# Kernel optimization log

Hardware: AMD Instinct MI355X
Metric: run time of the kernel (lower is better)

## Reference

```python
import jax, jax.numpy as jnp
import numpy as np

BATCH, DIM = 32, 512
STDDEV = 0.1


def _annihilation(dim):
    # diag(sqrt(1..dim-1), k=1), complex64
    d = jnp.sqrt(jnp.arange(1, dim, dtype=jnp.float32)).astype(jnp.complex64)
    return jnp.diag(d, k=1)


def setup_inputs() -> dict:
    key = jax.random.key(0)
    ks = jax.random.split(key, 8)
    f = lambda k, shape: jax.random.normal(k, shape, dtype=jnp.float32)
    return {
        'inputs_re': f(ks[0], (BATCH, DIM, DIM)),
        'inputs_im': f(ks[1], (BATCH, DIM, DIM)),
        'theta_1': f(ks[2], (1,)) * STDDEV,
        'theta_2': f(ks[3], (1,)) * STDDEV,
        'r': f(ks[4], (1,)) * STDDEV,
        'bx': f(ks[5], (1,)) * STDDEV,
        'bp': f(ks[6], (1,)) * STDDEV,
        'kappa': f(ks[7], (1,)) * STDDEV,
    }


def _forward(inputs_re, inputs_im, theta_1, theta_2, r, bx, bp, kappa):
    dim = inputs_re.shape[-1]
    x = jax.lax.complex(inputs_re, inputs_im)  # [B, dim, dim] complex64

    a = _annihilation(dim)                     # [dim, dim]
    a_dag = a.conj().T
    n_diag = jnp.arange(dim, dtype=jnp.float32).astype(jnp.complex64)  # number-operator diagonal

    # Rotation operators: expm(-1i*theta*N) with N diagonal -> closed-form diagonal exp (same math)
    th1 = theta_1[0].astype(jnp.complex64)
    th2 = theta_2[0].astype(jnp.complex64)
    R1 = jnp.diag(jnp.exp(-1j * th1 * n_diag))
    R2 = jnp.diag(jnp.exp(-1j * th2 * n_diag))

    # Kerr operator: expm(1i*kappa * (N*N elementwise)) ; N diagonal so N*N = diag(k^2)
    kap = kappa[0].astype(jnp.complex64)
    K = jnp.diag(jnp.exp(1j * kap * n_diag * n_diag))

    # Squeezing: in the TF source, '*' is ELEMENTWISE, and adjoint(a) (subdiag) elementwise
    # times a (superdiag) is the zero matrix -> generator is identically 0 -> S = expm(0) = I.
    # We keep the (zero) generator in the graph so r stays a (zero-grad) primal.
    r_c = r[0].astype(jnp.complex64)
    M_S = 0.5 * (r_c * (a_dag * a) - jnp.conj(r_c) * (a * a_dag))  # exactly zeros
    S = jnp.eye(dim, dtype=jnp.complex64) + M_S

    # Displacement: D = expm(alpha*a_dag - conj(alpha)*a). Generator M is skew-Hermitian,
    # so M = iH with H = -iM Hermitian; D = V diag(exp(i*w)) V^H via eigh (exact, differentiable).
    alpha = jax.lax.complex(bx[0], bp[0])
    M = alpha * a_dag - jnp.conj(alpha) * a
    H = (-1j) * M
    w, V = jnp.linalg.eigh(H)  # w real [dim], V [dim, dim]
    D = (V * jnp.exp(1j * w.astype(jnp.complex64))[None, :]) @ V.conj().T

    # Apply gates in the original order; operators are per-sample identical so
    # broadcast one [dim,dim] matrix over the batch instead of tiling.
    y = jnp.einsum('ij,bjk->bik', R1, x)
    y = jnp.einsum('ij,bjk->bik', S, y)
    y = jnp.einsum('ij,bjk->bik', R2, y)
    y = jnp.einsum('ij,bjk->bik', D, y)
    y = jnp.einsum('ij,bjk->bik', K, y)
    return y


def reference(inputs_re, inputs_im, theta_1, theta_2, r, bx, bp, kappa):
    return _forward(inputs_re, inputs_im, theta_1, theta_2, r, bx, bp, kappa)
```

## Files before the change

### kernel.cpp

```cpp
#include <hip/hip_runtime.h>
#include <hip/hip_fp16.h>

#define DIM 512
#define BATCH 32

typedef _Float16 half8 __attribute__((ext_vector_type(8)));
typedef float floatx4 __attribute__((ext_vector_type(4)));

static __device__ __forceinline__ unsigned short f2h(float f) {
    __half h = __float2half(f);
    return *reinterpret_cast<unsigned short*>(&h);
}

__global__ __launch_bounds__(256) void taylor_tables(const float* __restrict__ bxp,
                                                     const float* __restrict__ bpp,
                                                     const float* __restrict__ th1p,
                                                     const float* __restrict__ th2p,
                                                     const float* __restrict__ kapp,
                                                     float2* __restrict__ E,
                                                     float2* __restrict__ pm,
                                                     float2* __restrict__ pj) {
    if (blockIdx.x == 128) {
        for (int u = threadIdx.x; u < 2 * DIM; u += 256) {
            if (u < DIM) {
                float s, c;
                sincosf(kapp[0] * (float)(u * u), &s, &c);
                pm[u] = make_float2(c, s);
            } else {
                const int j = u - DIM;
                float s, c;
                sincosf(-(th1p[0] + th2p[0]) * (float)j, &s, &c);
                pj[j] = make_float2(c, s);
            }
        }
        return;
    }

    const int wave = (blockIdx.x * blockDim.x + threadIdx.x) >> 6;
    const int lane = threadIdx.x & 63;
    if (wave >= DIM) return;
    const int i = wave;
    const float bx = bxp[0], bp = bpp[0];
    const float invs = 0.5f;
    const int o = lane - 31;
    const int j = i + o;
    const bool jvalid = (j >= 0 && j < DIM);

    float pre = 0.f, pim = 0.f;
    if (o == -1 && i >= 1)      { float g = sqrtf((float)i)       * invs; pre =  bx * g; pim = bp * g; }
    if (o ==  1 && i + 1 < DIM) { float g = sqrtf((float)(i + 1)) * invs; pre = -bx * g; pim = bp * g; }
    float ere = (o == 0 ? 1.f : 0.f) + pre;
    float eim = pim;

    const float gs = (jvalid && j >= 1)       ? sqrtf((float)j)       * invs : 0.f;
    const float hs = (jvalid && j + 1 < DIM)  ? sqrtf((float)(j + 1)) * invs : 0.f;
    const float csup_re = -bx * gs, csup_im = bp * gs;
    const float csub_re =  bx * hs, csub_im = bp * hs;

    for (int k = 2; k <= 30; ++k) {
        const float invk = 1.f / (float)k;
        float pmre = __shfl_up(pre, 1, 64),   pmim = __shfl_up(pim, 1, 64);
        float ppre = __shfl_down(pre, 1, 64), ppim = __shfl_down(pim, 1, 64);
        if (lane == 0)  { pmre = 0.f; pmim = 0.f; }
        if (lane == 63) { ppre = 0.f; ppim = 0.f; }
        float nre = pmre * csup_re - pmim * csup_im + ppre * csub_re - ppim * csub_im;
        float nim = pmre * csup_im + pmim * csup_re + ppre * csub_im + ppim * csub_re;
        pre = nre * invk; pim = nim * invk;
        ere += pre; eim += pim;
    }

    for (int base = 0; base < DIM; base += 64) {
        const int c = base + lane;
        const int src = c - i + 31;
        const float tre = __shfl(ere, src & 63, 64);
        const float tim = __shfl(eim, src & 63, 64);
        float vre = 0.f, vim = 0.f;
        if (src >= 0 && src < 64) { vre = tre; vim = tim; }
        E[i * DIM + c] = make_float2(vre, vim);
    }
}

__global__ __launch_bounds__(256) void csq_fold32(const float2* __restrict__ A,
                                                  unsigned short* __restrict__ Gp,
                                                  const float2* __restrict__ pm,
                                                  const float2* __restrict__ pj) {
    __shared__ float2 At[16][33];
    __shared__ float2 Bt[16][33];
    const int j0 = blockIdx.x * 32, i0 = blockIdx.y * 32;
    const int tid = threadIdx.x;
    const int tx = tid & 15, ty = tid >> 4;
    const int lmin = max(0, max(i0, j0) - 32);
    const int lmax = min(DIM, min(i0, j0) + 64);

    float cre[2][2] = {{0.f}}, cim[2][2] = {{0.f}};
    for (int lt = lmin; lt < lmax; lt += 16) {
        for (int idx = tid; idx < 512; idx += 256) {
            const int r = idx >> 4, c = idx & 15;
            const int l = lt + c;
            At[c][r] = (l < lmax) ? A[(i0 + r) * DIM + l]       : make_float2(0.f, 0.f);
            Bt[c][r] = (l < lmax) ? A[(size_t)l * DIM + j0 + r] : make_float2(0.f, 0.f);
        }
        __syncthreads();
#pragma unroll
        for (int ll = 0; ll < 16; ++ll) {
            float2 a0 = At[ll][ty * 2], a1 = At[ll][ty * 2 + 1];
            float2 b0 = Bt[ll][tx * 2], b1 = Bt[ll][tx * 2 + 1];
            cre[0][0] += a0.x * b0.x - a0.y * b0.y;  cim[0][0] += a0.x * b0.y + a0.y * b0.x;
            cre[0][1] += a0.x * b1.x - a0.y * b1.y;  cim[0][1] += a0.x * b1.y + a0.y * b1.x;
            cre[1][0] += a1.x * b0.x - a1.y * b0.y;  cim[1][0] += a1.x * b0.y + a1.y * b0.x;
            cre[1][1] += a1.x * b1.x - a1.y * b1.y;  cim[1][1] += a1.x * b1.y + a1.y * b1.x;
        }
        __syncthreads();
    }

#pragma unroll
    for (int q = 0; q < 2; ++q) {
        const int m = i0 + ty * 2 + q;
        const float2 km = pm[m];
#pragma unroll
        for (int r = 0; r < 2; ++r) {
            const int j = j0 + tx * 2 + r;
            const float2 tj = pj[j];
            const float r1 = cre[q][r] * tj.x - cim[q][r] * tj.y;
            const float i1 = cre[q][r] * tj.y + cim[q][r] * tj.x;
            const float r2 = r1 * km.x - i1 * km.y;
            const float i2 = r1 * km.y + i1 * km.x;
            *reinterpret_cast<ushort2*>(Gp + (size_t)m * 1024 + 2 * j) =
                make_ushort2(f2h(r2), f2h(-i2));
        }
    }
}

#define XS_STRIDE 72
#define LDS_BARRIER()                                            \
    {                                                            \
        asm volatile("s_waitcnt lgkmcnt(0)" ::: "memory");       \
        __builtin_amdgcn_s_barrier();                            \
    }

__global__ __launch_bounds__(512, 4) void apply_fused(const unsigned short* __restrict__ Gp,
                                                      const float* __restrict__ xre,
                                                      const float* __restrict__ xim,
                                                      float* __restrict__ out) {
    __shared__ unsigned short Xs[2][128 * XS_STRIDE];

    const int k0 = blockIdx.x * 128, m0 = blockIdx.y * 128, b = blockIdx.z;
    const int tid = threadIdx.x, lane = tid & 63, w = tid >> 6;
    const int wr = w >> 1, wc = w & 1;
    const int lr = lane & 15, lk8 = (lane >> 4) * 8;

    const int jmin = max(0, m0 - 64);
    const int jmax = min(DIM, m0 + 192);
    const int nchunk = (jmax - jmin) >> 5;

    const int s_jl = (tid >> 3) & 31;
    const int s_kf = (tid >> 8) * 64 + (tid & 7) * 8;

    const unsigned short* gp = Gp + (size_t)(m0 + wr * 32 + lr) * 1024 + 2 * jmin + lk8;
    const size_t xrow0 = ((size_t)b * DIM + jmin + s_jl) * DIM + k0 + s_kf;

    floatx4 acc[2][4];
#pragma unroll
    for (int ms = 0; ms < 2; ++ms)
#pragma unroll
        for (int ns = 0; ns < 4; ++ns) {
            acc[ms][ns][0] = 0.f; acc[ms][ns][1] = 0.f;
            acc[ms][ns][2] = 0.f; acc[ms][ns][3] = 0.f;
        }

    float4 xrA[2], xiA[2], xrB[2], xiB[2];
    half8 ha[2][2];

#define LOADX(XR, XI, CH)                                                        \
    {                                                                            \
        const size_t xrow = xrow0 + (size_t)(CH) * 32 * DIM;                     \
        _Pragma("unroll")                                                        \
        for (int t = 0; t < 2; ++t) {                                            \
            XR[t] = *reinterpret_cast<const float4*>(xre + xrow + 4 * t);        \
            XI[t] = *reinterpret_cast<const float4*>(xim + xrow + 4 * t);        \
        }                                                                        \
    }

#define PACKC(XR, XI, BUF)                                                       \
    {                                                                            \
        _Pragma("unroll")                                                        \
        for (int t = 0; t < 2; ++t) {                                            \
            const int kb = s_kf + 4 * t;                                         \
            *reinterpret_cast<ushort2*>(&Xs[BUF][(kb + 0) * XS_STRIDE + 2 * s_jl]) = make_ushort2(f2h(XR[t].x), f2h(XI[t].x)); \
            *reinterpret_cast<ushort2*>(&Xs[BUF][(kb + 1) * XS_STRIDE + 2 * s_jl]) = make_ushort2(f2h(XR[t].y), f2h(XI[t].y)); \
            *reinterpret_cast<ushort2*>(&Xs[BUF][(kb + 2) * XS_STRIDE + 2 * s_jl]) = make_ushort2(f2h(XR[t].z), f2h(XI[t].z)); \
            *reinterpret_cast<ushort2*>(&Xs[BUF][(kb + 3) * XS_STRIDE + 2 * s_jl]) = make_ushort2(f2h(XR[t].w), f2h(XI[t].w)); \
        }                                                                        \
    }

#define LOADA(CH)                                                                \
    {                                                                            \
        _Pragma("unroll")                                                        \
        for (int s = 0; s < 2; ++s)                                              \
            _Pragma("unroll")                                                    \
            for (int ms = 0; ms < 2; ++ms)                                       \
                ha[s][ms] = *reinterpret_cast<const half8*>(gp + (size_t)ms * 16 * 1024 + (CH) * 64 + s * 32); \
    }

#define MFMA_BUF(BUF)                                                            \
    {                                                                            \
        const unsigned short* bbase = &Xs[BUF][(wc * 64 + lr) * XS_STRIDE + lk8];\
        __builtin_amdgcn_s_setprio(1);                                           \
        _Pragma("unroll")                                                        \
        for (int s = 0; s < 2; ++s) {                                            \
            half8 bb[4];                                                         \
            _Pragma("unroll")                                                    \
            for (int ns = 0; ns < 4; ++ns)                                       \
                bb[ns] = *reinterpret_cast<const half8*>(bbase + ns * 16 * XS_STRIDE + s * 32); \
            _Pragma("unroll")                                                    \
            for (int ms = 0; ms < 2; ++ms)                                       \
                _Pragma("unroll")                                                \
                for (int ns = 0; ns < 4; ++ns)                                   \
                    acc[ms][ns] = __builtin_amdgcn_mfma_f32_16x16x32_f16(ha[s][ms], bb[ns], acc[ms][ns], 0, 0, 0); \
        }                                                                        \
        __builtin_amdgcn_s_setprio(0);                                           \
    }

    LOADX(xrA, xiA, 0);
    LOADX(xrB, xiB, 1);
    PACKC(xrA, xiA, 0);
    LDS_BARRIER();

    for (int ch = 0; ch < nchunk; ch += 2) {
        LOADA(ch);
        if (ch + 2 < nchunk) LOADX(xrA, xiA, ch + 2);
        MFMA_BUF(0);
        PACKC(xrB, xiB, 1);
        LDS_BARRIER();
        LOADA(ch + 1);
        if (ch + 3 < nchunk) LOADX(xrB, xiB, ch + 3);
        MFMA_BUF(1);
        if (ch + 2 < nchunk) PACKC(xrA, xiA, 0);
        LDS_BARRIER();
    }

    float (*Ot)[65] = reinterpret_cast<float (*)[65]>(&Xs[0][0]);
    const int crow = (lane >> 4) * 4;
#pragma unroll
    for (int h = 0; h < 2; ++h) {
        if (wc == h) {
#pragma unroll
            for (int ms = 0; ms < 2; ++ms)
#pragma unroll
                for (int ns = 0; ns < 4; ++ns) {
                    const int kloc = ns * 16 + lr;
#pragma unroll
                    for (int e = 0; e < 4; ++e) {
                        const int mloc = wr * 32 + ms * 16 + crow + e;
                        Ot[mloc][kloc] = acc[ms][ns][e];
                    }
                }
        }
        LDS_BARRIER();
        const int klq = (tid & 15) * 4;
        const int kbase = k0 + h * 64 + klq;
#pragma unroll
        for (int i = 0; i < 4; ++i) {
            const int mr = (tid >> 4) + 32 * i;
            float4 v;
            v.x = Ot[mr][klq + 0];
            v.y = Ot[mr][klq + 1];
            v.z = Ot[mr][klq + 2];
            v.w = Ot[mr][klq + 3];
            *reinterpret_cast<float4*>(out + ((size_t)b * DIM + m0 + mr) * DIM + kbase) = v;
        }
        LDS_BARRIER();
    }
#undef LOADX
#undef PACKC
#undef LOADA
#undef MFMA_BUF
}

extern "C" void kernel_launch(void* const* d_in, const int* in_sizes, int n_in,
                              void* d_out, int out_size, void* d_ws, size_t ws_size,
                              hipStream_t stream) {
    const float* xre = (const float*)d_in[0];
    const float* xim = (const float*)d_in[1];
    const float* th1 = (const float*)d_in[2];
    const float* th2 = (const float*)d_in[3];
    const float* bx  = (const float*)d_in[5];
    const float* bp  = (const float*)d_in[6];
    const float* kap = (const float*)d_in[7];
    float* out = (float*)d_out;

    char* ws = (char*)d_ws;
    float2* E           = (float2*)ws;
    unsigned short* Gp  = (unsigned short*)(ws + 2u * 1024 * 1024);
    float2* pm          = (float2*)(ws + 3u * 1024 * 1024);
    float2* pj          = pm + DIM;

    hipLaunchKernelGGL(taylor_tables, dim3(129), dim3(256), 0, stream,
                       bx, bp, th1, th2, kap, E, pm, pj);
    hipLaunchKernelGGL(csq_fold32, dim3(16, 16), dim3(256), 0, stream,
                       E, Gp, pm, pj);
    hipLaunchKernelGGL(apply_fused, dim3(4, 4, BATCH), dim3(512), 0, stream,
                       Gp, xre, xim, out);
}
```

Measured before the change: 51.99 us.

## Stream fp32 X tiles directly to LDS via global_load_lds and convert at MFMA time

Replaces the register-staged load, fp16 pack and LDS store of the input tile with direct global-to-LDS transfers of raw fp32 real and imaginary rows. The fp16 conversion moves into the MFMA phase using packed round-toward-zero conversion. This is meant to remove the VGPR staging and transpose-store cost and to overlap the next chunk's transfer via vmcnt waits. In exchange LDS use doubles (fp32), occupancy drops to 2 waves per SIMD, the loop is single-chunk with two barriers per chunk, and each MFMA operand now needs eight scalar LDS reads plus conversions.

Result: slower. 54.31 us (+4.5%).

```diff
diff --git a/kernel.cpp b/kernel.cpp
--- a/kernel.cpp
+++ b/kernel.cpp
@@ -10,6 +10,11 @@
 static __device__ __forceinline__ unsigned short f2h(float f) {
     __half h = __float2half(f);
     return *reinterpret_cast<unsigned short*>(&h);
+}
+
+static __device__ __forceinline__ unsigned int pkrtz(float a, float b) {
+    auto v = __builtin_amdgcn_cvt_pkrtz(a, b);
+    return __builtin_bit_cast(unsigned int, v);
 }
 
 __global__ __launch_bounds__(256) void taylor_tables(const float* __restrict__ bxp,
@@ -131,33 +136,23 @@
     }
 }
 
-#define XS_STRIDE 72
-#define LDS_BARRIER()                                            \
-    {                                                            \
-        asm volatile("s_waitcnt lgkmcnt(0)" ::: "memory");       \
-        __builtin_amdgcn_s_barrier();                            \
-    }
-
-__global__ __launch_bounds__(512, 4) void apply_fused(const unsigned short* __restrict__ Gp,
+#define PAIR_STRIDE 1040
+__global__ __launch_bounds__(512, 2) void apply_fused(const unsigned short* __restrict__ Gp,
                                                       const float* __restrict__ xre,
                                                       const float* __restrict__ xim,
                                                       float* __restrict__ out) {
-    __shared__ unsigned short Xs[2][128 * XS_STRIDE];
+    __shared__ __align__(16) char smem[2][2][16 * PAIR_STRIDE];
 
     const int k0 = blockIdx.x * 128, m0 = blockIdx.y * 128, b = blockIdx.z;
     const int tid = threadIdx.x, lane = tid & 63, w = tid >> 6;
     const int wr = w >> 1, wc = w & 1;
-    const int lr = lane & 15, lk8 = (lane >> 4) * 8;
+    const int lr = lane & 15, lq = lane >> 4, lk8 = lq * 8;
 
     const int jmin = max(0, m0 - 64);
     const int jmax = min(DIM, m0 + 192);
     const int nchunk = (jmax - jmin) >> 5;
 
-    const int s_jl = (tid >> 3) & 31;
-    const int s_kf = (tid >> 8) * 64 + (tid & 7) * 8;
-
     const unsigned short* gp = Gp + (size_t)(m0 + wr * 32 + lr) * 1024 + 2 * jmin + lk8;
-    const size_t xrow0 = ((size_t)b * DIM + jmin + s_jl) * DIM + k0 + s_kf;
 
     floatx4 acc[2][4];
 #pragma unroll
@@ -168,28 +163,23 @@
             acc[ms][ns][2] = 0.f; acc[ms][ns][3] = 0.f;
         }
 
-    float4 xrA[2], xiA[2], xrB[2], xiB[2];
     half8 ha[2][2];
 
-#define LOADX(XR, XI, CH)                                                        \
-    {                                                                            \
-        const size_t xrow = xrow0 + (size_t)(CH) * 32 * DIM;                     \
-        _Pragma("unroll")                                                        \
-        for (int t = 0; t < 2; ++t) {                                            \
-            XR[t] = *reinterpret_cast<const float4*>(xre + xrow + 4 * t);        \
-            XI[t] = *reinterpret_cast<const float4*>(xim + xrow + 4 * t);        \
-        }                                                                        \
-    }
-
-#define PACKC(XR, XI, BUF)                                                       \
+#define DMA(CH, BUF)                                                             \
     {                                                                            \
         _Pragma("unroll")                                                        \
-        for (int t = 0; t < 2; ++t) {                                            \
-            const int kb = s_kf + 4 * t;                                         \
-            *reinterpret_cast<ushort2*>(&Xs[BUF][(kb + 0) * XS_STRIDE + 2 * s_jl]) = make_ushort2(f2h(XR[t].x), f2h(XI[t].x)); \
-            *reinterpret_cast<ushort2*>(&Xs[BUF][(kb + 1) * XS_STRIDE + 2 * s_jl]) = make_ushort2(f2h(XR[t].y), f2h(XI[t].y)); \
-            *reinterpret_cast<ushort2*>(&Xs[BUF][(kb + 2) * XS_STRIDE + 2 * s_jl]) = make_ushort2(f2h(XR[t].z), f2h(XI[t].z)); \
-            *reinterpret_cast<ushort2*>(&Xs[BUF][(kb + 3) * XS_STRIDE + 2 * s_jl]) = make_ushort2(f2h(XR[t].w), f2h(XI[t].w)); \
+        for (int i = 0; i < 2; ++i) {                                            \
+            const int p = i * 8 + w;                                             \
+            const size_t grow = ((size_t)b * DIM + jmin + (CH) * 32 + p * 2 +    \
+                                 (lane >> 5)) * DIM + k0 + (lane & 31) * 4;      \
+            __builtin_amdgcn_global_load_lds(                                    \
+                (const __attribute__((address_space(1))) void*)(xre + grow),     \
+                (__attribute__((address_space(3))) void*)(&smem[BUF][0][p * PAIR_STRIDE]), \
+                16, 0, 0);                                                       \
+            __builtin_amdgcn_global_load_lds(                                    \
+                (const __attribute__((address_space(1))) void*)(xim + grow),     \
+                (__attribute__((address_space(3))) void*)(&smem[BUF][1][p * PAIR_STRIDE]), \
+                16, 0, 0);                                                       \
         }                                                                        \
     }
 
@@ -202,45 +192,52 @@
                 ha[s][ms] = *reinterpret_cast<const half8*>(gp + (size_t)ms * 16 * 1024 + (CH) * 64 + s * 32); \
     }
 
-#define MFMA_BUF(BUF)                                                            \
+#define MFMA_PHASE(BUF)                                                          \
     {                                                                            \
-        const unsigned short* bbase = &Xs[BUF][(wc * 64 + lr) * XS_STRIDE + lk8];\
+        const char* xreL = smem[BUF][0];                                         \
+        const char* ximL = smem[BUF][1];                                         \
         __builtin_amdgcn_s_setprio(1);                                           \
         _Pragma("unroll")                                                        \
-        for (int s = 0; s < 2; ++s) {                                            \
-            half8 bb[4];                                                         \
+        for (int s = 0; s < 2; ++s)                                              \
             _Pragma("unroll")                                                    \
-            for (int ns = 0; ns < 4; ++ns)                                       \
-                bb[ns] = *reinterpret_cast<const half8*>(bbase + ns * 16 * XS_STRIDE + s * 32); \
-            _Pragma("unroll")                                                    \
-            for (int ms = 0; ms < 2; ++ms)                                       \
+            for (int ns = 0; ns < 4; ++ns) {                                     \
+                const int kcol = wc * 64 + ns * 16 + lr;                         \
+                union { half8 h; unsigned int u32[4]; } u;                       \
                 _Pragma("unroll")                                                \
-                for (int ns = 0; ns < 4; ++ns)                                   \
-                    acc[ms][ns] = __builtin_amdgcn_mfma_f32_16x16x32_f16(ha[s][ms], bb[ns], acc[ms][ns], 0, 0, 0); \
-        }                                                                        \
+                for (int jj = 0; jj < 4; ++jj) {                                 \
+                    const int j = s * 16 + lq * 4 + jj;                          \
+                    const int off = (j >> 1) * PAIR_STRIDE + (j & 1) * 512 + kcol * 4; \
+                    const float re = *reinterpret_cast<const float*>(xreL + off);\
+                    const float im = *reinterpret_cast<const float*>(ximL + off);\
+                    u.u32[jj] = pkrtz(re, im);                                   \
+                }                                                                \
+                _Pragma("unroll")                                                \
+                for (int ms = 0; ms < 2; ++ms)                                   \
+                    acc[ms][ns] = __builtin_amdgcn_mfma_f32_16x16x32_f16(ha[s][ms], u.h, acc[ms][ns], 0, 0, 0); \
+            }                                                                    \
         __builtin_amdgcn_s_setprio(0);                                           \
     }
 
-    LOADX(xrA, xiA, 0);
-    LOADX(xrB, xiB, 1);
-    PACKC(xrA, xiA, 0);
-    LDS_BARRIER();
-
-    for (int ch = 0; ch < nchunk; ch += 2) {
+    DMA(0, 0);
+
+    for (int ch = 0; ch < nchunk; ++ch) {
         LOADA(ch);
-        if (ch + 2 < nchunk) LOADX(xrA, xiA, ch + 2);
-        MFMA_BUF(0);
-        PACKC(xrB, xiB, 1);
-        LDS_BARRIER();
-        LOADA(ch + 1);
-        if (ch + 3 < nchunk) LOADX(xrB, xiB, ch + 3);
-        MFMA_BUF(1);
-        if (ch + 2 < nchunk) PACKC(xrA, xiA, 0);
-        LDS_BARRIER();
-    }
-
-    float (*Ot)[65] = reinterpret_cast<float (*)[65]>(&Xs[0][0]);
-    const int crow = (lane >> 4) * 4;
+        __builtin_amdgcn_sched_barrier(0);
+        if (ch + 1 < nchunk) {
+            DMA(ch + 1, (ch + 1) & 1);
+            __builtin_amdgcn_sched_barrier(0);
+            asm volatile("s_waitcnt vmcnt(4)" ::: "memory");
+        } else {
+            asm volatile("s_waitcnt vmcnt(0)" ::: "memory");
+        }
+        __builtin_amdgcn_s_barrier();
+        MFMA_PHASE(ch & 1);
+        asm volatile("" ::: "memory");
+        __builtin_amdgcn_s_barrier();
+    }
+
+    float (*Ot)[65] = reinterpret_cast<float (*)[65]>(&smem[0][0][0]);
+    const int crow = lq * 4;
 #pragma unroll
     for (int h = 0; h < 2; ++h) {
         if (wc == h) {
@@ -256,7 +253,8 @@
                     }
                 }
         }
-        LDS_BARRIER();
+        asm volatile("s_waitcnt lgkmcnt(0)" ::: "memory");
+        __builtin_amdgcn_s_barrier();
         const int klq = (tid & 15) * 4;
         const int kbase = k0 + h * 64 + klq;
 #pragma unroll
@@ -269,12 +267,12 @@
             v.w = Ot[mr][klq + 3];
             *reinterpret_cast<float4*>(out + ((size_t)b * DIM + m0 + mr) * DIM + kbase) = v;
         }
-        LDS_BARRIER();
-    }
-#undef LOADX
-#undef PACKC
+        asm volatile("s_waitcnt lgkmcnt(0)" ::: "memory");
+        __builtin_amdgcn_s_barrier();
+    }
+#undef DMA
 #undef LOADA
-#undef MFMA_BUF
+#undef MFMA_PHASE
 }
 
 extern "C" void kernel_launch(void* const* d_in, const int* in_sizes, int n_in,
```
